# Kernel optimization log

Measured on AMD Instinct MI355X. Metric: run time of the kernel, lower is better.

Reference implementation:

```python
import jax, jax.numpy as jnp
import numpy as np

KERNEL_SIZE = 5
DILATION = 2
DYNAMIC_SIZE = 24


def setup_inputs() -> dict:
    key = jax.random.key(0)
    k1, k2 = jax.random.split(key)
    B, C, P, H, W = 4, 32, 8, 512, 512
    inp = jax.random.normal(k1, (B, C, H, W), dtype=jnp.float32)
    params = jax.random.normal(k2, (B, P, H, W), dtype=jnp.float32)
    return {"input": inp, "params": params}


def _pixel_bilateral_filter(inp, params, kernel_size, dilation):
    """Per-pixel bilateral filter.

    For each pixel, gathers a kernel_size x kernel_size dilated neighborhood,
    computes range weights w = exp(-||params_center - params_neighbor||^2)
    (zero weight for out-of-bounds taps), and returns the normalized weighted
    sum of the input. Vectorized over B/H/W; the only Python loop is over the
    k*k static tap offsets, avoiding an im2col intermediate.
    """
    B, C, H, W = inp.shape
    half = kernel_size // 2
    pad = half * dilation
    pad_cfg = ((0, 0), (0, 0), (pad, pad), (pad, pad))
    inp_p = jnp.pad(inp, pad_cfg)          # [B,C,H+2p,W+2p], zero pad
    par_p = jnp.pad(params, pad_cfg)       # [B,P,H+2p,W+2p]
    mask_p = jnp.pad(jnp.ones((B, 1, H, W), inp.dtype), pad_cfg)  # validity

    acc = jnp.zeros_like(inp)
    wsum = jnp.zeros((B, 1, H, W), inp.dtype)
    for dy in range(kernel_size):
        for dx in range(kernel_size):
            oy, ox = dy * dilation, dx * dilation
            pn = par_p[:, :, oy:oy + H, ox:ox + W]   # neighbor guide features
            mn = mask_p[:, :, oy:oy + H, ox:ox + W]  # 1 if in-bounds
            d2 = jnp.sum((params - pn) ** 2, axis=1, keepdims=True)  # [B,1,H,W]
            w = mn * jnp.exp(-d2)
            acc = acc + w * inp_p[:, :, oy:oy + H, ox:ox + W]
            wsum = wsum + w
    return acc / (wsum + jnp.asarray(1e-8, inp.dtype))


def reference(input, params):
    out = _pixel_bilateral_filter(input, params, KERNEL_SIZE, DILATION)
    return out[:, 0:DYNAMIC_SIZE, :, :]
```

## Files before the change

### kernel.cpp

```cpp
#include <hip/hip_runtime.h>

#define KS   5
#define DIL  2
#define PAD  4
#define B_   4
#define C_   32
#define P_   8
#define OUTC 24
#define H_   512
#define W_   512
#define HW   (H_ * W_)
#define NP   (P_ + OUTC)
#define LROW 528

typedef float2 f2;

__global__ __launch_bounds__(256, 4)
void bilateral_db(const float* __restrict__ inp,
                  const float* __restrict__ par,
                  float* __restrict__ out)
{
    __shared__ float lds[2][KS][LROW];

    const int nwg = gridDim.x;
    const int bid = blockIdx.x;
    const int sb  = (bid & 7) * (nwg >> 3) + (bid >> 3);
    const int b = sb >> 9;
    const int y = sb & (H_ - 1);

    const int u  = threadIdx.x;
    const int x0 = u << 1;

    const float* __restrict__ parb = par + (size_t)b * P_ * HW;
    const float* __restrict__ inpb = inp + (size_t)b * C_ * HW;
    float* __restrict__ outb       = out + (size_t)b * OUTC * HW;

    int  rowoff[KS];
    bool rowok[KS];
#pragma unroll
    for (int d = 0; d < KS; ++d) {
        const int yy = y + d * DIL - PAD;
        rowok[d]  = (yy >= 0) & (yy < H_);
        rowoff[d] = min(max(yy, 0), H_ - 1) * W_;
    }

    if (u < 8) {
        const int bi = u >> 2, col = u & 3;
#pragma unroll
        for (int r = 0; r < KS; ++r) {
            lds[bi][r][col] = 0.f;
            lds[bi][r][516 + col] = 0.f;
        }
    }

    f2 stg[KS];
    auto issue = [&](int t) {
        const float* plane = (t < P_) ? (parb + (size_t)t * HW)
                                      : (inpb + (size_t)(t - P_) * HW);
#pragma unroll
        for (int r = 0; r < KS; ++r)
            stg[r] = *(const f2*)(plane + rowoff[r] + x0);
    };
    auto commit = [&](int bi) {
#pragma unroll
        for (int r = 0; r < KS; ++r)
            *(f2*)&lds[bi][r][4 + x0] = stg[r];
    };

    f2 d2[KS * KS];
#pragma unroll
    for (int d = 0; d < KS; ++d) {
#pragma unroll
        for (int e = 0; e < KS; ++e) {
            const int xb = x0 + e * DIL - PAD;
            d2[d * KS + e].x = (rowok[d] && (xb + 0 >= 0) && (xb + 0 < W_)) ? 0.f : 1e5f;
            d2[d * KS + e].y = (rowok[d] && (xb + 1 >= 0) && (xb + 1 < W_)) ? 0.f : 1e5f;
        }
    }

    issue(0);
    commit(0);
    issue(1);

#pragma unroll 1
    for (int t = 0; t < P_; ++t) {
        __syncthreads();
        commit((t + 1) & 1);
        issue(t + 2);
        const int bi = t & 1;
        const f2 pc = *(const f2*)&lds[bi][2][4 + x0];
#pragma unroll
        for (int d = 0; d < KS; ++d) {
#pragma unroll
            for (int e = 0; e < KS; ++e) {
                if (d == 2 && e == 2) continue;
                const f2 v = *(const f2*)&lds[bi][d][x0 + 2 * e];
                const float tx = pc.x - v.x;
                const float ty = pc.y - v.y;
                d2[d * KS + e].x += tx * tx;
                d2[d * KS + e].y += ty * ty;
            }
        }
    }

    f2 w[KS * KS];
    float sx = 0.f, sy = 0.f;
#pragma unroll
    for (int q = 0; q < KS * KS; ++q) {
        w[q].x = __expf(-d2[q].x);
        w[q].y = __expf(-d2[q].y);
        sx += w[q].x;
        sy += w[q].y;
    }
    const float ivx = 1.f / (sx + 1e-8f);
    const float ivy = 1.f / (sy + 1e-8f);

    const size_t obase = (size_t)y * W_ + x0;
#pragma unroll 1
    for (int t = P_; t < NP; ++t) {
        __syncthreads();
        if (t + 1 < NP) {
            commit((t + 1) & 1);
            if (t + 2 < NP) issue(t + 2);
        }
        const int bi = t & 1;
        float ax = 0.f, ay = 0.f;
#pragma unroll
        for (int d = 0; d < KS; ++d) {
#pragma unroll
            for (int e = 0; e < KS; ++e) {
                const f2 v = *(const f2*)&lds[bi][d][x0 + 2 * e];
                ax += w[d * KS + e].x * v.x;
                ay += w[d * KS + e].y * v.y;
            }
        }
        f2 o;
        o.x = ax * ivx;
        o.y = ay * ivy;
        *(f2*)(outb + (size_t)(t - P_) * HW + obase) = o;
    }
}

extern "C" void kernel_launch(void* const* d_in, const int* in_sizes, int n_in,
                              void* d_out, int out_size, void* d_ws, size_t ws_size,
                              hipStream_t stream) {
    const float* inp = (const float*)d_in[0];
    const float* par = (const float*)d_in[1];
    float* out = (float*)d_out;

    dim3 block(256);
    dim3 grid(B_ * H_);
    bilateral_db<<<grid, block, 0, stream>>>(inp, par, out);
}
```

Baseline: 268.4 us.

## Process four pixels per thread with float4 LDS reads and shuffled taps

Each thread now handles four adjacent output pixels instead of two, and the block shrinks to 128 threads. Each row's neighbourhood comes from three float4 LDS reads, and the odd-offset taps are built by register shuffles, which cuts LDS read instructions per output. The normalisation is folded into the weights before the channel loop, and the commit/issue of the next plane moves after the compute. The cost is more registers (100 weight floats per thread) and fewer threads per block, which may lower occupancy.

```diff
diff --git a/kernel.cpp b/kernel.cpp
--- a/kernel.cpp
+++ b/kernel.cpp
@@ -13,10 +13,14 @@
 #define NP   (P_ + OUTC)
 #define LROW 528
 
-typedef float2 f2;
+typedef float4 f4;
 
-__global__ __launch_bounds__(256, 4)
-void bilateral_db(const float* __restrict__ inp,
+__device__ __forceinline__ f4 s2(const f4 a, const f4 b) {
+    return make_float4(a.z, a.w, b.x, b.y);
+}
+
+__global__ __launch_bounds__(128, 3)
+void bilateral_w4(const float* __restrict__ inp,
                   const float* __restrict__ par,
                   float* __restrict__ out)
 {
@@ -29,7 +33,7 @@
     const int y = sb & (H_ - 1);
 
     const int u  = threadIdx.x;
-    const int x0 = u << 1;
+    const int x0 = u << 2;
 
     const float* __restrict__ parb = par + (size_t)b * P_ * HW;
     const float* __restrict__ inpb = inp + (size_t)b * C_ * HW;
@@ -53,92 +57,133 @@
         }
     }
 
-    f2 stg[KS];
+    f4 stg[KS];
     auto issue = [&](int t) {
-        const float* plane = (t < P_) ? (parb + (size_t)t * HW)
-                                      : (inpb + (size_t)(t - P_) * HW);
+        const float* pl = (t < P_) ? (parb + (size_t)t * HW)
+                                   : (inpb + (size_t)(t - P_) * HW);
 #pragma unroll
         for (int r = 0; r < KS; ++r)
-            stg[r] = *(const f2*)(plane + rowoff[r] + x0);
+            stg[r] = *(const f4*)(pl + rowoff[r] + x0);
     };
     auto commit = [&](int bi) {
 #pragma unroll
         for (int r = 0; r < KS; ++r)
-            *(f2*)&lds[bi][r][4 + x0] = stg[r];
+            *(f4*)&lds[bi][r][4 + x0] = stg[r];
     };
 
-    f2 d2[KS * KS];
+    f4 wd[KS * KS];
 #pragma unroll
     for (int d = 0; d < KS; ++d) {
 #pragma unroll
         for (int e = 0; e < KS; ++e) {
             const int xb = x0 + e * DIL - PAD;
-            d2[d * KS + e].x = (rowok[d] && (xb + 0 >= 0) && (xb + 0 < W_)) ? 0.f : 1e5f;
-            d2[d * KS + e].y = (rowok[d] && (xb + 1 >= 0) && (xb + 1 < W_)) ? 0.f : 1e5f;
+            f4 v;
+            v.x = (rowok[d] && (xb + 0 >= 0) && (xb + 0 < W_)) ? 0.f : 1e5f;
+            v.y = (rowok[d] && (xb + 1 >= 0) && (xb + 1 < W_)) ? 0.f : 1e5f;
+            v.z = (rowok[d] && (xb + 2 >= 0) && (xb + 2 < W_)) ? 0.f : 1e5f;
+            v.w = (rowok[d] && (xb + 3 >= 0) && (xb + 3 < W_)) ? 0.f : 1e5f;
+            wd[d * KS + e] = v;
         }
     }
 
-    issue(0);
-    commit(0);
-    issue(1);
+#define WACC(t_, T_) do {                                   \
+        float dx_;                                          \
+        dx_ = pc.x - (T_).x; wd[t_].x += dx_ * dx_;         \
+        dx_ = pc.y - (T_).y; wd[t_].y += dx_ * dx_;         \
+        dx_ = pc.z - (T_).z; wd[t_].z += dx_ * dx_;         \
+        dx_ = pc.w - (T_).w; wd[t_].w += dx_ * dx_;         \
+    } while (0)
+
+#define CACC(t_, T_) do {                                   \
+        acc.x += wd[t_].x * (T_).x;                         \
+        acc.y += wd[t_].y * (T_).y;                         \
+        acc.z += wd[t_].z * (T_).z;                         \
+        acc.w += wd[t_].w * (T_).w;                         \
+    } while (0)
+
+    issue(0); commit(0); issue(1);
 
 #pragma unroll 1
     for (int t = 0; t < P_; ++t) {
         __syncthreads();
+        const int bi = t & 1;
+
+        const f4 r2c0 = *(const f4*)&lds[bi][2][x0];
+        const f4 r2c1 = *(const f4*)&lds[bi][2][x0 + 4];
+        const f4 r2c2 = *(const f4*)&lds[bi][2][x0 + 8];
+        const f4 pc = r2c1;
+        {
+            const f4 t1 = s2(r2c0, r2c1), t3 = s2(r2c1, r2c2);
+            WACC(2 * KS + 0, r2c0);
+            WACC(2 * KS + 1, t1);
+            WACC(2 * KS + 3, t3);
+            WACC(2 * KS + 4, r2c2);
+        }
+#pragma unroll
+        for (int dd = 0; dd < 4; ++dd) {
+            const int d = (dd < 2) ? dd : dd + 1;
+            const f4 c0 = *(const f4*)&lds[bi][d][x0];
+            const f4 c1 = *(const f4*)&lds[bi][d][x0 + 4];
+            const f4 c2 = *(const f4*)&lds[bi][d][x0 + 8];
+            const f4 t1 = s2(c0, c1), t3 = s2(c1, c2);
+            WACC(d * KS + 0, c0);
+            WACC(d * KS + 1, t1);
+            WACC(d * KS + 2, c1);
+            WACC(d * KS + 3, t3);
+            WACC(d * KS + 4, c2);
+        }
+
         commit((t + 1) & 1);
         issue(t + 2);
-        const int bi = t & 1;
-        const f2 pc = *(const f2*)&lds[bi][2][4 + x0];
+    }
+
+    {
+        float sx = 0.f, sy = 0.f, sz = 0.f, sw = 0.f;
 #pragma unroll
-        for (int d = 0; d < KS; ++d) {
+        for (int q = 0; q < KS * KS; ++q) {
+            wd[q].x = __expf(-wd[q].x);
+            wd[q].y = __expf(-wd[q].y);
+            wd[q].z = __expf(-wd[q].z);
+            wd[q].w = __expf(-wd[q].w);
+            sx += wd[q].x; sy += wd[q].y; sz += wd[q].z; sw += wd[q].w;
+        }
+        const float ivx = 1.f / (sx + 1e-8f);
+        const float ivy = 1.f / (sy + 1e-8f);
+        const float ivz = 1.f / (sz + 1e-8f);
+        const float ivw = 1.f / (sw + 1e-8f);
 #pragma unroll
-            for (int e = 0; e < KS; ++e) {
-                if (d == 2 && e == 2) continue;
-                const f2 v = *(const f2*)&lds[bi][d][x0 + 2 * e];
-                const float tx = pc.x - v.x;
-                const float ty = pc.y - v.y;
-                d2[d * KS + e].x += tx * tx;
-                d2[d * KS + e].y += ty * ty;
-            }
+        for (int q = 0; q < KS * KS; ++q) {
+            wd[q].x *= ivx; wd[q].y *= ivy; wd[q].z *= ivz; wd[q].w *= ivw;
         }
     }
-
-    f2 w[KS * KS];
-    float sx = 0.f, sy = 0.f;
-#pragma unroll
-    for (int q = 0; q < KS * KS; ++q) {
-        w[q].x = __expf(-d2[q].x);
-        w[q].y = __expf(-d2[q].y);
-        sx += w[q].x;
-        sy += w[q].y;
-    }
-    const float ivx = 1.f / (sx + 1e-8f);
-    const float ivy = 1.f / (sy + 1e-8f);
 
     const size_t obase = (size_t)y * W_ + x0;
 #pragma unroll 1
     for (int t = P_; t < NP; ++t) {
         __syncthreads();
+        const int bi = t & 1;
+        f4 acc = make_float4(0.f, 0.f, 0.f, 0.f);
+#pragma unroll
+        for (int d = 0; d < KS; ++d) {
+            const f4 c0 = *(const f4*)&lds[bi][d][x0];
+            const f4 c1 = *(const f4*)&lds[bi][d][x0 + 4];
+            const f4 c2 = *(const f4*)&lds[bi][d][x0 + 8];
+            const f4 t1 = s2(c0, c1), t3 = s2(c1, c2);
+            CACC(d * KS + 0, c0);
+            CACC(d * KS + 1, t1);
+            CACC(d * KS + 2, c1);
+            CACC(d * KS + 3, t3);
+            CACC(d * KS + 4, c2);
+        }
+        *(f4*)(outb + (size_t)(t - P_) * HW + obase) = acc;
+
         if (t + 1 < NP) {
             commit((t + 1) & 1);
             if (t + 2 < NP) issue(t + 2);
         }
-        const int bi = t & 1;
-        float ax = 0.f, ay = 0.f;
-#pragma unroll
-        for (int d = 0; d < KS; ++d) {
-#pragma unroll
-            for (int e = 0; e < KS; ++e) {
-                const f2 v = *(const f2*)&lds[bi][d][x0 + 2 * e];
-                ax += w[d * KS + e].x * v.x;
-                ay += w[d * KS + e].y * v.y;
-            }
-        }
-        f2 o;
-        o.x = ax * ivx;
-        o.y = ay * ivy;
-        *(f2*)(outb + (size_t)(t - P_) * HW + obase) = o;
     }
+#undef WACC
+#undef CACC
 }
 
 extern "C" void kernel_launch(void* const* d_in, const int* in_sizes, int n_in,
@@ -148,7 +193,7 @@
     const float* par = (const float*)d_in[1];
     float* out = (float*)d_out;
 
-    dim3 block(256);
+    dim3 block(128);
     dim3 grid(B_ * H_);
-    bilateral_db<<<grid, block, 0, stream>>>(inp, par, out);
+    bilateral_w4<<<grid, block, 0, stream>>>(inp, par, out);
 }
```

After: 421.7 us. 57.1% more time.
